# Kernel optimization log

Hardware: AMD Instinct MI355X
Metric: run time of the kernel (lower is better)

The kernel has to match this reference:

```python
import jax, jax.numpy as jnp
import numpy as np

RADIUS = 1.3
COARSE = 32          # coarse_reso
FINE = 2             # fine_reso[0]
NUM_ATOMS = 32
SH_DIM = 9           # (sh_deg+1)^2, sh_deg=2
DATA_DIM = SH_DIM * 3 + 1  # 28
BATCH = 512
N_INT = COARSE * 3 * 2 * FINE  # 384 intersections per ray

# 8 trilinear neighbor offsets, same order as the torch module
_OFFSETS = jnp.array([[-1, -1, -1], [-1, -1, 1], [-1, 1, -1], [-1, 1, 1],
                      [1, -1, -1], [1, -1, 1], [1, 1, -1], [1, 1, 1]], dtype=jnp.float32)


def sh_encode(d):
    """Real spherical harmonics basis, degree 2 (9 components), on normalized dirs."""
    d = d / jnp.linalg.norm(d, axis=-1, keepdims=True)
    x, y, z = d[..., 0], d[..., 1], d[..., 2]
    c0 = 0.28209479177387814
    c1 = 0.48860251190291987
    c2a = 1.0925484305920792
    c2b = 0.31539156525252005
    c2c = 0.5462742152960396
    return jnp.stack([
        c0 * jnp.ones_like(x),
        -c1 * y, c1 * z, -c1 * x,
        c2a * x * y, -c2a * y * z,
        c2b * (2.0 * z * z - x * x - y * y),
        -c2a * x * z,
        c2c * (x * x - y * y)], axis=-1)


def dict_interp(pts, grid, atoms):
    """Multi-res voxel trilinear gather + dictionary-atom accumulate.
    pts: [N,3] world coords; grid: [COARSE^3, A]; atoms: [FINE^3, A, D]."""
    fine_vlen = (2.0 * RADIUS / COARSE) / FINE
    p = (pts + RADIUS) / fine_vlen                       # [N,3] fine-grid coords
    pre = p[:, None, :] + _OFFSETS[None] / 2.0           # [N,8,3]
    post = jnp.clip(jnp.floor(pre), 0.0, COARSE * FINE - 1)
    offs = jnp.abs(p[:, None, :] - (post + 0.5))         # [N,8,3]
    w = jnp.prod(1.0 - offs, axis=-1)                    # [N,8] trilinear weights
    idx = post.astype(jnp.int32)
    c = idx // FINE                                      # coarse cell per-axis
    f = idx % FINE                                       # fine cell per-axis
    cflat = (c[..., 0] * COARSE + c[..., 1]) * COARSE + c[..., 2]  # [N,8]
    fflat = (f[..., 0] * FINE + f[..., 1]) * FINE + f[..., 2]      # [N,8]
    out = jnp.zeros((pts.shape[0], DATA_DIM), pts.dtype)
    for n in range(8):
        cv = grid[cflat[:, n]]                           # [N,A] gathered coarse weights
        av = atoms[fflat[:, n]]                          # [N,A,D] gathered atoms
        out = out + w[:, n, None] * jnp.einsum('na,nad->nd', cv, av)
    return out


def setup_inputs() -> dict:
    key = jax.random.key(0)
    k1, k2, k3, k4 = jax.random.split(key, 4)
    rays_o = jax.random.uniform(k1, (BATCH, 3), jnp.float32, -0.5, 0.5)
    rays_d = jax.random.normal(k2, (BATCH, 3), jnp.float32)
    rays_d = rays_d / jnp.linalg.norm(rays_d, axis=-1, keepdims=True)
    grid = 0.01 * jax.random.normal(k3, (COARSE ** 3, NUM_ATOMS), jnp.float32)
    atoms = jnp.concatenate([
        jax.random.uniform(k4, (FINE ** 3, NUM_ATOMS, DATA_DIM - 1), jnp.float32),
        jnp.full((FINE ** 3, NUM_ATOMS, 1), 0.01, jnp.float32)], axis=-1)
    return {"rays_o": rays_o, "rays_d": rays_d, "grid": grid, "atoms": atoms, "grid_id": 0}


def reference(rays_o, rays_d, grid, atoms, grid_id):
    del grid_id  # single scene
    step = ((2.0 * RADIUS / COARSE) / FINE) / 2.0
    # sample_proposal (no_grad in the original)
    off_pos = (RADIUS - rays_o) / rays_d
    off_neg = (-RADIUS - rays_o) / rays_d
    start = jnp.max(jnp.minimum(off_pos, off_neg), axis=-1, keepdims=True)
    steps = jnp.arange(N_INT, dtype=rays_o.dtype)[None]
    intersections = jax.lax.stop_gradient(start + steps * step)  # [B, N_INT]
    ts = intersections[:, :-1]                                    # [B, S]
    pts = jax.lax.stop_gradient(
        rays_o[:, None, :] + ts[..., None] * rays_d[:, None, :])  # [B,S,3]
    mask = jnp.all((pts > -RADIUS) & (pts < RADIUS), axis=-1)     # [B,S]
    B, S = ts.shape
    data = dict_interp(pts.reshape(-1, 3), grid, atoms).reshape(B, S, DATA_DIM)
    # masked_scatter_ equivalent: zero out out-of-box samples
    sigma = jnp.where(mask, jax.nn.relu(data[..., -1]), 0.0)
    dists = (intersections[:, 1:] - intersections[:, :-1]) * jnp.linalg.norm(rays_d, axis=-1, keepdims=True)
    alpha = 1.0 - jnp.exp(-sigma * dists)
    T = jnp.cumprod(1.0 - alpha + 1e-10, axis=-1)
    T = jnp.concatenate([jnp.ones_like(T[:, :1]), T[:, :-1]], axis=-1)
    abs_light = alpha * T                                         # [B,S]
    sh = sh_encode(rays_d)                                        # [B,SH_DIM]
    sh_vals = data[..., :-1].reshape(B, S, 3, SH_DIM)
    rgb_s = jnp.einsum('bk,bsck->bsc', sh, sh_vals)               # [B,S,3]
    rgb_s = jnp.where(mask[..., None], rgb_s, 0.0)
    rgb = jnp.sum(abs_light[..., None] * jax.nn.sigmoid(rgb_s), axis=1)
    rgb = rgb + (1.0 - jnp.sum(abs_light, axis=-1, keepdims=True))  # white background
    depth = jnp.sum(abs_light * ts, axis=-1)
    consistency_loss = jnp.zeros((), rgb.dtype)  # noise_std == 0
    return rgb, alpha, depth, consistency_loss
```

## Files before the change

kernel.cpp:

```cpp
#include <hip/hip_runtime.h>
#include <math.h>

#define R_ 1.3f
#define NCOARSE 32
#define SAMPLES 383
#define BATCH 512
#define STEPSZ 0.0203125f
#define INV_FINE_VLEN 24.615384615384617f

using f32x4 = __attribute__((ext_vector_type(4))) float;
using s16x8 = __attribute__((ext_vector_type(8))) short;
using u32x4 = __attribute__((ext_vector_type(4))) unsigned int;
using bf16x2 = __attribute__((ext_vector_type(2))) __bf16;

__device__ __forceinline__ unsigned int packbf2(float lo, float hi) {
    bf16x2 v;
    v.x = (__bf16)lo;
    v.y = (__bf16)hi;
    return __builtin_bit_cast(unsigned int, v);
}

__device__ __forceinline__ void dimwc(float p, float* W, int* C) {
    float post0 = fminf(fmaxf(floorf(p - 0.5f), 0.f), 63.f);
    float post1 = fminf(fmaxf(floorf(p + 0.5f), 0.f), 63.f);
    float w0 = 1.f - fabsf(p - (post0 + 0.5f));
    float w1 = 1.f - fabsf(p - (post1 + 0.5f));
    int i0 = (int)post0, i1 = (int)post1;
    int f0 = i0 & 1, f1 = i1 & 1;
    W[0] = (f0 == 0 ? w0 : 0.f) + (f1 == 0 ? w1 : 0.f);
    W[1] = (f0 == 1 ? w0 : 0.f) + (f1 == 1 ? w1 : 0.f);
    int c0 = i0 >> 1, c1 = i1 >> 1;
    C[0] = (f0 == 0) ? c0 : c1;
    C[1] = (f0 == 1) ? c0 : c1;
}

__global__ __launch_bounds__(512, 4) void dp_fused(
    const float* __restrict__ rays_o, const float* __restrict__ rays_d,
    const float* __restrict__ grid, const float* __restrict__ atoms,
    float* __restrict__ out_rgb, float* __restrict__ out_alpha,
    float* __restrict__ out_depth, float* __restrict__ out_loss)
{
    __shared__ u32x4 Bf[16][64];
    __shared__ u32x4 Abuf[8][256];
    __shared__ float alpha_l[384];
    __shared__ float sig_l[384][3];
    __shared__ float segtot[8];
    __shared__ float part[6][5];

    const int b = blockIdx.x;
    const int tid = threadIdx.x;
    const int wid = tid >> 6, l = tid & 63;
    const int sl = l & 15, fp = l >> 4;

    const int s0i = tid, s1i = tid + 512;
    const int ll0 = s0i & 63, nt0 = (s0i >> 6) & 1, kb0 = s0i >> 7;
    const int ll1 = s1i & 63, nt1 = (s1i >> 6) & 1, kb1 = s1i >> 7;
    const int a00 = (ll0 >> 4) * 8, d0 = nt0 * 16 + (ll0 & 15);
    const int a01 = (ll1 >> 4) * 8, d1 = nt1 * 16 + (ll1 & 15);
    float la0[8], la1[8];
#pragma unroll
    for (int j = 0; j < 8; ++j) {
        la0[j] = (d0 < 28) ? atoms[(kb0 * 32 + a00 + j) * 28 + d0] : 0.f;
        la1[j] = (d1 < 28) ? atoms[(kb1 * 32 + a01 + j) * 28 + d1] : 0.f;
    }

    if (b == 0 && tid == 0) out_loss[0] = 0.f;

    if (tid < 384) alpha_l[tid] = 0.f;
    {
        float* sf = &sig_l[0][0];
        for (int i = tid; i < 384 * 3; i += 512) sf[i] = 0.f;
    }

    const float ox = rays_o[3 * b], oy = rays_o[3 * b + 1], oz = rays_o[3 * b + 2];
    const float dx = rays_d[3 * b], dy = rays_d[3 * b + 1], dz = rays_d[3 * b + 2];
    const float start = fmaxf(fmaxf(
        fminf((R_ - ox) / dx, (-R_ - ox) / dx),
        fminf((R_ - oy) / dy, (-R_ - oy) / dy)),
        fminf((R_ - oz) / dz, (-R_ - oz) / dz));
    const float t_exit = fminf(fminf(
        fmaxf((R_ - ox) / dx, (-R_ - ox) / dx),
        fmaxf((R_ - oy) / dy, (-R_ - oy) / dy)),
        fmaxf((R_ - oz) / dz, (-R_ - oz) / dz));
    const int ns = (int)floorf((t_exit - start) / STEPSZ) + 2;
    const int ntiles = min(24, (ns >> 4) + 2);

    const float lend = sqrtf(dx * dx + dy * dy + dz * dz);
    const float dist = STEPSZ * lend;
    const float inv = 1.f / lend;
    const float nx = dx * inv, ny = dy * inv, nz = dz * inv;
    float sh[9];
    sh[0] = 0.28209479177387814f;
    sh[1] = -0.48860251190291987f * ny;
    sh[2] = 0.48860251190291987f * nz;
    sh[3] = -0.48860251190291987f * nx;
    sh[4] = 1.0925484305920792f * nx * ny;
    sh[5] = -1.0925484305920792f * ny * nz;
    sh[6] = 0.31539156525252005f * (2.f * nz * nz - nx * nx - ny * ny);
    sh[7] = -1.0925484305920792f * nx * nz;
    sh[8] = 0.5462742152960396f * (nx * nx - ny * ny);

    {
        u32x4 o0, o1;
#pragma unroll
        for (int e2 = 0; e2 < 4; ++e2) {
            o0[e2] = packbf2(la0[2 * e2], la0[2 * e2 + 1]);
            o1[e2] = packbf2(la1[2 * e2], la1[2 * e2 + 1]);
        }
        Bf[s0i >> 6][ll0] = o0;
        Bf[s1i >> 6][ll1] = o1;
    }

    __syncthreads();

    u32x4* W4 = &Abuf[wid][0];
    float* Dbuf = (float*)W4;

    for (int t = wid; t < ntiles; t += 8) {
        const int s = t * 16 + sl;
        const float tt = start + s * STEPSZ;
        const float px = ox + tt * dx, py = oy + tt * dy, pz = oz + tt * dz;
        const bool m = (s < SAMPLES) &&
                       (px > -R_ && px < R_ && py > -R_ && py < R_ && pz > -R_ && pz < R_);
        if (__ballot(m) == 0ull) continue;

        float W0[2], W1[2], W2[2];
        int C0[2], C1[2], C2[2];
        dimwc((px + R_) * INV_FINE_VLEN, W0, C0);
        dimwc((py + R_) * INV_FINE_VLEN, W1, C1);
        dimwc((pz + R_) * INV_FINE_VLEN, W2, C2);
        const float msk = m ? 1.f : 0.f;

        const int f0c = fp, f1c = 4 + fp;
        const float wf0 = msk * W0[(f0c >> 2) & 1] * W1[(f0c >> 1) & 1] * W2[f0c & 1];
        const float wf1 = msk * W0[(f1c >> 2) & 1] * W1[(f1c >> 1) & 1] * W2[f1c & 1];
        const int cf0 = (C0[(f0c >> 2) & 1] * NCOARSE + C1[(f0c >> 1) & 1]) * NCOARSE + C2[f0c & 1];
        const int cf1 = (C0[(f1c >> 2) & 1] * NCOARSE + C1[(f1c >> 1) & 1]) * NCOARSE + C2[f1c & 1];
        const f32x4* gr0 = (const f32x4*)(grid + cf0 * 32);
        const f32x4* gr1 = (const f32x4*)(grid + cf1 * 32);

        f32x4 q0 = gr1[0], q1 = gr1[1], q2 = gr1[2], q3 = gr1[3];
        f32x4 q4 = gr1[4], q5 = gr1[5], q6 = gr1[6], q7 = gr1[7];

        f32x4 acc0 = {0.f, 0.f, 0.f, 0.f};
        f32x4 acc1 = {0.f, 0.f, 0.f, 0.f};

#pragma unroll
        for (int g4 = 0; g4 < 4; ++g4) {
            const f32x4 v0 = gr0[2 * g4];
            const f32x4 v1 = gr0[2 * g4 + 1];
            u32x4 o;
            o.x = packbf2(wf0 * v0.x, wf0 * v0.y);
            o.y = packbf2(wf0 * v0.z, wf0 * v0.w);
            o.z = packbf2(wf0 * v1.x, wf0 * v1.y);
            o.w = packbf2(wf0 * v1.z, wf0 * v1.w);
            W4[fp * 64 + 16 * g4 + sl] = o;
        }
#pragma unroll
        for (int kb2 = 0; kb2 < 4; ++kb2) {
            const s16x8 af = __builtin_bit_cast(s16x8, W4[kb2 * 64 + l]);
            acc0 = __builtin_amdgcn_mfma_f32_16x16x32_bf16(
                af, __builtin_bit_cast(s16x8, Bf[kb2 * 2 + 0][l]), acc0, 0, 0, 0);
            acc1 = __builtin_amdgcn_mfma_f32_16x16x32_bf16(
                af, __builtin_bit_cast(s16x8, Bf[kb2 * 2 + 1][l]), acc1, 0, 0, 0);
        }
        {
            u32x4 o;
            o.x = packbf2(wf1 * q0.x, wf1 * q0.y);
            o.y = packbf2(wf1 * q0.z, wf1 * q0.w);
            o.z = packbf2(wf1 * q1.x, wf1 * q1.y);
            o.w = packbf2(wf1 * q1.z, wf1 * q1.w);
            W4[fp * 64 + sl] = o;
            o.x = packbf2(wf1 * q2.x, wf1 * q2.y);
            o.y = packbf2(wf1 * q2.z, wf1 * q2.w);
            o.z = packbf2(wf1 * q3.x, wf1 * q3.y);
            o.w = packbf2(wf1 * q3.z, wf1 * q3.w);
            W4[fp * 64 + 16 + sl] = o;
            o.x = packbf2(wf1 * q4.x, wf1 * q4.y);
            o.y = packbf2(wf1 * q4.z, wf1 * q4.w);
            o.z = packbf2(wf1 * q5.x, wf1 * q5.y);
            o.w = packbf2(wf1 * q5.z, wf1 * q5.w);
            W4[fp * 64 + 32 + sl] = o;
            o.x = packbf2(wf1 * q6.x, wf1 * q6.y);
            o.y = packbf2(wf1 * q6.z, wf1 * q6.w);
            o.z = packbf2(wf1 * q7.x, wf1 * q7.y);
            o.w = packbf2(wf1 * q7.z, wf1 * q7.w);
            W4[fp * 64 + 48 + sl] = o;
        }
#pragma unroll
        for (int kb2 = 0; kb2 < 4; ++kb2) {
            const s16x8 af = __builtin_bit_cast(s16x8, W4[kb2 * 64 + l]);
            acc0 = __builtin_amdgcn_mfma_f32_16x16x32_bf16(
                af, __builtin_bit_cast(s16x8, Bf[(4 + kb2) * 2 + 0][l]), acc0, 0, 0, 0);
            acc1 = __builtin_amdgcn_mfma_f32_16x16x32_bf16(
                af, __builtin_bit_cast(s16x8, Bf[(4 + kb2) * 2 + 1][l]), acc1, 0, 0, 0);
        }

#pragma unroll
        for (int r = 0; r < 4; ++r) {
            Dbuf[(4 * fp + r) * 33 + sl]      = acc0[r];
            Dbuf[(4 * fp + r) * 33 + sl + 16] = acc1[r];
        }

        const int s2 = l >> 2, c = l & 3;
        const int so = t * 16 + s2;
        if (c == 3) {
            const float sigma = fmaxf(Dbuf[s2 * 33 + 27], 0.f);
            alpha_l[so] = 1.f - __expf(-sigma * dist);
        } else {
            float r_ = 0.f;
#pragma unroll
            for (int k = 0; k < 9; ++k) r_ += sh[k] * Dbuf[s2 * 33 + c * 9 + k];
            sig_l[so][c] = __builtin_amdgcn_rcpf(1.f + __expf(-r_));
        }
    }

    __syncthreads();

    if (tid < SAMPLES) out_alpha[b * SAMPLES + tid] = alpha_l[tid];

    float a_s = 0.f, incl = 1.f;
    if (wid < 6) {
        const int s = wid * 64 + l;
        const bool v = s < SAMPLES;
        a_s = v ? alpha_l[s] : 0.f;
        incl = v ? (1.f - a_s + 1e-10f) : 1.f;
#pragma unroll
        for (int off = 1; off < 64; off <<= 1) {
            const float tm = __shfl_up(incl, off, 64);
            if (l >= off) incl *= tm;
        }
        if (l == 63) segtot[wid] = incl;
    }
    __syncthreads();
    if (wid < 6) {
        float pre = 1.f;
        for (int k = 0; k < wid; ++k) pre *= segtot[k];
        float excl = __shfl_up(incl, 1, 64);
        if (l == 0) excl = 1.f;
        const int s = wid * 64 + l;
        const bool v = s < SAMPLES;
        const float al = v ? a_s * pre * excl : 0.f;
        float r0 = al * sig_l[s][0];
        float r1 = al * sig_l[s][1];
        float r2 = al * sig_l[s][2];
        float sd = al * (start + s * STEPSZ);
        float sa = al;
#pragma unroll
        for (int m2 = 32; m2 > 0; m2 >>= 1) {
            r0 += __shfl_xor(r0, m2, 64);
            r1 += __shfl_xor(r1, m2, 64);
            r2 += __shfl_xor(r2, m2, 64);
            sd += __shfl_xor(sd, m2, 64);
            sa += __shfl_xor(sa, m2, 64);
        }
        if (l == 0) {
            part[wid][0] = r0; part[wid][1] = r1; part[wid][2] = r2;
            part[wid][3] = sd; part[wid][4] = sa;
        }
    }
    __syncthreads();
    if (tid == 0) {
        float r0 = 0.f, r1 = 0.f, r2 = 0.f, sd = 0.f, sa = 0.f;
#pragma unroll
        for (int j = 0; j < 6; ++j) {
            r0 += part[j][0]; r1 += part[j][1]; r2 += part[j][2];
            sd += part[j][3]; sa += part[j][4];
        }
        const float base = 1.f - sa;
        out_rgb[b * 3 + 0] = r0 + base;
        out_rgb[b * 3 + 1] = r1 + base;
        out_rgb[b * 3 + 2] = r2 + base;
        out_depth[b] = sd;
    }
}

extern "C" void kernel_launch(void* const* d_in, const int* in_sizes, int n_in,
                              void* d_out, int out_size, void* d_ws, size_t ws_size,
                              hipStream_t stream) {
    const float* rays_o = (const float*)d_in[0];
    const float* rays_d = (const float*)d_in[1];
    const float* grid   = (const float*)d_in[2];
    const float* atoms  = (const float*)d_in[3];
    float* out   = (float*)d_out;
    float* rgb   = out;
    float* alpha = out + BATCH * 3;
    float* depth = out + BATCH * 3 + BATCH * SAMPLES;
    float* loss  = out + BATCH * 3 + BATCH * SAMPLES + BATCH;

    dp_fused<<<dim3(BATCH), dim3(512), 0, stream>>>(
        rays_o, rays_d, grid, atoms, rgb, alpha, depth, loss);
}
```

Measured before the change: 17.27 us.

## Build MFMA A-operand directly in registers instead of staging through LDS

Each lane now gathers its own 8-element slice of the grid row for all 8 fine corners and packs the bf16 A fragment in registers, feeding it straight into the MFMA. This removes the per-wave LDS write/read round trip (Abuf) used to transpose the gathered grid values. LDS per wave shrinks to the D-output scratch. Global loads become narrower per lane (two 16-byte loads per corner, 8 corners) rather than full rows per lane, which changes coalescing and the number of load instructions.

```diff
diff --git a/kernel.cpp b/kernel.cpp
--- a/kernel.cpp
+++ b/kernel.cpp
@@ -41,7 +41,7 @@
     float* __restrict__ out_depth, float* __restrict__ out_loss)
 {
     __shared__ u32x4 Bf[16][64];
-    __shared__ u32x4 Abuf[8][256];
+    __shared__ float Dw[8][544];
     __shared__ float alpha_l[384];
     __shared__ float sig_l[384][3];
     __shared__ float segtot[8];
@@ -50,7 +50,7 @@
     const int b = blockIdx.x;
     const int tid = threadIdx.x;
     const int wid = tid >> 6, l = tid & 63;
-    const int sl = l & 15, fp = l >> 4;
+    const int sl = l & 15, j8 = (l >> 4) * 8;
 
     const int s0i = tid, s1i = tid + 512;
     const int ll0 = s0i & 63, nt0 = (s0i >> 6) & 1, kb0 = s0i >> 7;
@@ -113,8 +113,7 @@
 
     __syncthreads();
 
-    u32x4* W4 = &Abuf[wid][0];
-    float* Dbuf = (float*)W4;
+    float* Dbuf = &Dw[wid][0];
 
     for (int t = wid; t < ntiles; t += 8) {
         const int s = t * 16 + sl;
@@ -131,71 +130,41 @@
         dimwc((pz + R_) * INV_FINE_VLEN, W2, C2);
         const float msk = m ? 1.f : 0.f;
 
-        const int f0c = fp, f1c = 4 + fp;
-        const float wf0 = msk * W0[(f0c >> 2) & 1] * W1[(f0c >> 1) & 1] * W2[f0c & 1];
-        const float wf1 = msk * W0[(f1c >> 2) & 1] * W1[(f1c >> 1) & 1] * W2[f1c & 1];
-        const int cf0 = (C0[(f0c >> 2) & 1] * NCOARSE + C1[(f0c >> 1) & 1]) * NCOARSE + C2[f0c & 1];
-        const int cf1 = (C0[(f1c >> 2) & 1] * NCOARSE + C1[(f1c >> 1) & 1]) * NCOARSE + C2[f1c & 1];
-        const f32x4* gr0 = (const f32x4*)(grid + cf0 * 32);
-        const f32x4* gr1 = (const f32x4*)(grid + cf1 * 32);
-
-        f32x4 q0 = gr1[0], q1 = gr1[1], q2 = gr1[2], q3 = gr1[3];
-        f32x4 q4 = gr1[4], q5 = gr1[5], q6 = gr1[6], q7 = gr1[7];
-
         f32x4 acc0 = {0.f, 0.f, 0.f, 0.f};
         f32x4 acc1 = {0.f, 0.f, 0.f, 0.f};
 
 #pragma unroll
-        for (int g4 = 0; g4 < 4; ++g4) {
-            const f32x4 v0 = gr0[2 * g4];
-            const f32x4 v1 = gr0[2 * g4 + 1];
-            u32x4 o;
-            o.x = packbf2(wf0 * v0.x, wf0 * v0.y);
-            o.y = packbf2(wf0 * v0.z, wf0 * v0.w);
-            o.z = packbf2(wf0 * v1.x, wf0 * v1.y);
-            o.w = packbf2(wf0 * v1.z, wf0 * v1.w);
-            W4[fp * 64 + 16 * g4 + sl] = o;
-        }
-#pragma unroll
-        for (int kb2 = 0; kb2 < 4; ++kb2) {
-            const s16x8 af = __builtin_bit_cast(s16x8, W4[kb2 * 64 + l]);
-            acc0 = __builtin_amdgcn_mfma_f32_16x16x32_bf16(
-                af, __builtin_bit_cast(s16x8, Bf[kb2 * 2 + 0][l]), acc0, 0, 0, 0);
-            acc1 = __builtin_amdgcn_mfma_f32_16x16x32_bf16(
-                af, __builtin_bit_cast(s16x8, Bf[kb2 * 2 + 1][l]), acc1, 0, 0, 0);
-        }
-        {
-            u32x4 o;
-            o.x = packbf2(wf1 * q0.x, wf1 * q0.y);
-            o.y = packbf2(wf1 * q0.z, wf1 * q0.w);
-            o.z = packbf2(wf1 * q1.x, wf1 * q1.y);
-            o.w = packbf2(wf1 * q1.z, wf1 * q1.w);
-            W4[fp * 64 + sl] = o;
-            o.x = packbf2(wf1 * q2.x, wf1 * q2.y);
-            o.y = packbf2(wf1 * q2.z, wf1 * q2.w);
-            o.z = packbf2(wf1 * q3.x, wf1 * q3.y);
-            o.w = packbf2(wf1 * q3.z, wf1 * q3.w);
-            W4[fp * 64 + 16 + sl] = o;
-            o.x = packbf2(wf1 * q4.x, wf1 * q4.y);
-            o.y = packbf2(wf1 * q4.z, wf1 * q4.w);
-            o.z = packbf2(wf1 * q5.x, wf1 * q5.y);
-            o.w = packbf2(wf1 * q5.z, wf1 * q5.w);
-            W4[fp * 64 + 32 + sl] = o;
-            o.x = packbf2(wf1 * q6.x, wf1 * q6.y);
-            o.y = packbf2(wf1 * q6.z, wf1 * q6.w);
-            o.z = packbf2(wf1 * q7.x, wf1 * q7.y);
-            o.w = packbf2(wf1 * q7.z, wf1 * q7.w);
-            W4[fp * 64 + 48 + sl] = o;
-        }
-#pragma unroll
-        for (int kb2 = 0; kb2 < 4; ++kb2) {
-            const s16x8 af = __builtin_bit_cast(s16x8, W4[kb2 * 64 + l]);
-            acc0 = __builtin_amdgcn_mfma_f32_16x16x32_bf16(
-                af, __builtin_bit_cast(s16x8, Bf[(4 + kb2) * 2 + 0][l]), acc0, 0, 0, 0);
-            acc1 = __builtin_amdgcn_mfma_f32_16x16x32_bf16(
-                af, __builtin_bit_cast(s16x8, Bf[(4 + kb2) * 2 + 1][l]), acc1, 0, 0, 0);
-        }
-
+        for (int half = 0; half < 2; ++half) {
+            f32x4 qa[4], qb[4];
+            float wf[4];
+#pragma unroll
+            for (int k2 = 0; k2 < 4; ++k2) {
+                const int kb = half * 4 + k2;
+                const int fx = (kb >> 2) & 1, fy = (kb >> 1) & 1, fz = kb & 1;
+                wf[k2] = msk * W0[fx] * W1[fy] * W2[fz];
+                const int cf = (C0[fx] * NCOARSE + C1[fy]) * NCOARSE + C2[fz];
+                const f32x4* gp = (const f32x4*)(grid + cf * 32 + j8);
+                qa[k2] = gp[0];
+                qb[k2] = gp[1];
+            }
+#pragma unroll
+            for (int k2 = 0; k2 < 4; ++k2) {
+                const int kb = half * 4 + k2;
+                const float w = wf[k2];
+                u32x4 o;
+                o.x = packbf2(w * qa[k2].x, w * qa[k2].y);
+                o.y = packbf2(w * qa[k2].z, w * qa[k2].w);
+                o.z = packbf2(w * qb[k2].x, w * qb[k2].y);
+                o.w = packbf2(w * qb[k2].z, w * qb[k2].w);
+                const s16x8 af = __builtin_bit_cast(s16x8, o);
+                acc0 = __builtin_amdgcn_mfma_f32_16x16x32_bf16(
+                    af, __builtin_bit_cast(s16x8, Bf[kb * 2 + 0][l]), acc0, 0, 0, 0);
+                acc1 = __builtin_amdgcn_mfma_f32_16x16x32_bf16(
+                    af, __builtin_bit_cast(s16x8, Bf[kb * 2 + 1][l]), acc1, 0, 0, 0);
+            }
+        }
+
+        const int fp = l >> 4;
 #pragma unroll
         for (int r = 0; r < 4; ++r) {
             Dbuf[(4 * fp + r) * 33 + sl]      = acc0[r];
```

New measurement: 16.99 us. No clear change (-1.6%).
